# Kernel optimization log

Measured on AMD Instinct MI355X. Metric: run time of the kernel, lower is better.

Reference implementation:

```python
import jax, jax.numpy as jnp
import numpy as np
import itertools
from jax import lax

B, CIN, COUT, RES, NH = 32, 512, 512, 56, 8
STRIDE = RES // 7  # 8 -> post-stride grid is 7x7 (N=49)
HD = COUT // NH    # 64


def _affine(x, s, b):  # BatchNorm2d in inference form (per-channel scale/shift)
    return x * s[None, :, None, None] + b[None, :, None, None]


def _conv1x1(x, w):  # w: [O, C]
    return jnp.einsum('oc,bchw->bohw', w, x)


def _conv3x3(x, w, stride, groups):
    return lax.conv_general_dilated(
        x, w, window_strides=(stride, stride), padding=[(1, 1), (1, 1)],
        feature_group_count=groups, dimension_numbers=('NCHW', 'OIHW', 'NCHW'))


def _bias_idx():
    points = list(itertools.product(range(7), range(7)))
    offsets, idxs = {}, []
    for p1 in points:
        for p2 in points:
            off = (abs(p1[0] - p2[0]), abs(p1[1] - p2[1]))
            if off not in offsets:
                offsets[off] = len(offsets)
            idxs.append(offsets[off])
    return np.array(idxs, dtype=np.int32).reshape(49, 49), len(offsets)


def setup_inputs() -> dict:
    key = jax.random.key(0)
    ks = jax.random.split(key, 24)
    idx_np, n_off = _bias_idx()  # n_off = 49
    rn = lambda k, sh, sc: jax.random.normal(k, sh, dtype=jnp.float32) * sc
    return {
        'x': rn(ks[0], (B, CIN, RES, RES), 1.0),
        'dw_w': rn(ks[1], (CIN, 1, 3, 3), 0.2),
        'bn0_s': 1.0 + rn(ks[2], (CIN,), 0.05), 'bn0_b': rn(ks[3], (CIN,), 0.05),
        'wq': rn(ks[4], (COUT, CIN), 0.03),
        'bnq_s': 1.0 + rn(ks[5], (COUT,), 0.05), 'bnq_b': rn(ks[6], (COUT,), 0.05),
        'wk': rn(ks[7], (COUT, CIN), 0.03),
        'bnk_s': 1.0 + rn(ks[8], (COUT,), 0.05), 'bnk_b': rn(ks[9], (COUT,), 0.05),
        'wv': rn(ks[10], (COUT, CIN), 0.03),
        'bnv_s': 1.0 + rn(ks[11], (COUT,), 0.05), 'bnv_b': rn(ks[12], (COUT,), 0.05),
        'loc_w': rn(ks[13], (COUT, COUT // NH, 3, 3), 0.05), 'loc_b': rn(ks[14], (COUT,), 0.02),
        'bnl_s': 1.0 + rn(ks[15], (COUT,), 0.05), 'bnl_b': rn(ks[16], (COUT,), 0.05),
        'th1': rn(ks[17], (NH, NH), 0.3), 'th2': rn(ks[18], (NH, NH), 0.3),
        'logit_scale': jnp.log(10.0) * jnp.ones((NH, 1, 1), dtype=jnp.float32),
        'ab': rn(ks[19], (NH, n_off), 0.02),
        'wo': rn(ks[20], (COUT, COUT), 0.03),
        'bno_s': 1.0 + rn(ks[21], (COUT,), 0.05), 'bno_b': rn(ks[22], (COUT,), 0.05),
        'bias_idx': jnp.array(idx_np),
    }


def reference(x, dw_w, bn0_s, bn0_b, wq, bnq_s, bnq_b, wk, bnk_s, bnk_b,
              wv, bnv_s, bnv_b, loc_w, loc_b, bnl_s, bnl_b, th1, th2,
              logit_scale, ab, wo, bno_s, bno_b, bias_idx):
    # stride_conv: depthwise 3x3 stride-8 + BN -> [B, C, 7, 7]
    x = _affine(_conv3x3(x, dw_w, STRIDE, CIN), bn0_s, bn0_b)
    Bc, C, H, W = x.shape
    N = H * W  # 49
    q = _affine(_conv1x1(x, wq), bnq_s, bnq_b).reshape(Bc, NH, HD, N).transpose(0, 1, 3, 2)  # [B,H,N,d]
    k = _affine(_conv1x1(x, wk), bnk_s, bnk_b).reshape(Bc, NH, HD, N)                        # [B,H,d,N]
    v4 = _affine(_conv1x1(x, wv), bnv_s, bnv_b)                                              # [B,Cout,7,7]
    v_local = _affine(_conv3x3(v4, loc_w, 1, NH) + loc_b[None, :, None, None], bnl_s, bnl_b)
    v = v4.reshape(Bc, NH, HD, N).transpose(0, 1, 3, 2)                                      # [B,H,N,d]
    # faithful to source: q normalized over head_dim, k normalized over token axis (last)
    qn = q / jnp.maximum(jnp.linalg.norm(q, axis=-1, keepdims=True), 1e-12)
    kn = k / jnp.maximum(jnp.linalg.norm(k, axis=-1, keepdims=True), 1e-12)
    ls = jnp.exp(jnp.minimum(logit_scale, jnp.log(100.0)))  # clamp max then exp
    attn = jnp.einsum('bhnd,bhdm->bhnm', qn, kn) * ls + ab[:, bias_idx]  # [B,H,49,49]
    attn = jnp.einsum('ij,bjnm->binm', th1, attn)   # talking head 1
    attn = jax.nn.softmax(attn, axis=-1)
    attn = jnp.einsum('ij,bjnm->binm', th2, attn)   # talking head 2
    out = jnp.einsum('bhnm,bhmd->bhnd', attn, v)    # [B,H,N,d]
    out = out.transpose(0, 1, 3, 2).reshape(Bc, COUT, H, W) + v_local
    out = jax.image.resize(out, (Bc, COUT, H * STRIDE, W * STRIDE), method='bilinear')
    out = out * jax.nn.relu6(out + 3.0) / 6.0       # Hardswish
    return _affine(_conv1x1(out, wo), bno_s, bno_b)
```

## Files before the change

### kernel.cpp

```cpp
#include <hip/hip_runtime.h>
#include <hip/hip_bf16.h>
#include <stdint.h>

typedef short short8 __attribute__((ext_vector_type(8)));
typedef float f32x4 __attribute__((ext_vector_type(4)));

#define NB    32
#define NC    512
#define NHD   8
#define HDD   64
#define N7    49
#define RES   56
#define P56   3136
#define NTOK  1568
#define NTOKP 1664
#define NBIG  100352
#define KDIM  512
#define KLOC  576

__device__ __forceinline__ void gload_lds16(const __hip_bfloat16* g, __hip_bfloat16* l) {
  __builtin_amdgcn_global_load_lds(
      (const __attribute__((address_space(1))) void*)g,
      (__attribute__((address_space(3))) void*)l, 16, 0, 0);
}

__global__ __launch_bounds__(256) void k_cvt(
    const float* __restrict__ s0, const float* __restrict__ s1,
    const float* __restrict__ s2, const float* __restrict__ s3,
    const float* __restrict__ s4,
    __hip_bfloat16* __restrict__ d0, __hip_bfloat16* __restrict__ d1,
    __hip_bfloat16* __restrict__ d2, __hip_bfloat16* __restrict__ d3,
    __hip_bfloat16* __restrict__ d4) {
  const float* s; __hip_bfloat16* d; int n = NC * NC;
  switch (blockIdx.y) {
    case 0: s = s0; d = d0; break;
    case 1: s = s1; d = d1; break;
    case 2: s = s2; d = d2; break;
    case 3: s = s3; d = d3; break;
    default: s = s4; d = d4; n = NC * KLOC; break;
  }
  for (int i = blockIdx.x * blockDim.x + threadIdx.x; i < n; i += gridDim.x * blockDim.x)
    d[i] = __float2bfloat16(s[i]);
}

__global__ __launch_bounds__(64) void k_stride(
    const float* __restrict__ x, const float* __restrict__ dw,
    const float* __restrict__ s0, const float* __restrict__ b0,
    __hip_bfloat16* __restrict__ xs) {
  const int ci = blockIdx.x, b = blockIdx.y, t = threadIdx.x;
  __shared__ float rows[21][56];
  const float* xp = x + ((size_t)(b * NC + ci)) * RES * RES;
  for (int r = t; r < 21 * 56; r += 64) {
    int rr = r / 56, cc = r - rr * 56;
    int oh = rr / 3, kh = rr - oh * 3;
    int ih = oh * 8 + kh - 1;
    rows[rr][cc] = (ih >= 0) ? xp[ih * 56 + cc] : 0.f;
  }
  float w[9];
#pragma unroll
  for (int j = 0; j < 9; ++j) w[j] = dw[ci * 9 + j];
  const float sc = s0[ci], bi = b0[ci];
  __syncthreads();
  if (t < 49) {
    const int oh = t / 7, ow = t - oh * 7;
    float acc = 0.f;
#pragma unroll
    for (int kh = 0; kh < 3; ++kh)
#pragma unroll
      for (int kw = 0; kw < 3; ++kw) {
        int col = ow * 8 + kw - 1;
        float v = (col >= 0) ? rows[oh * 3 + kh][col] : 0.f;
        acc += v * w[kh * 3 + kw];
      }
    xs[(size_t)(b * 49 + t) * NC + ci] = __float2bfloat16(acc * sc + bi);
  }
}

__global__ __launch_bounds__(512) void k_gemm_big(
    const __hip_bfloat16* __restrict__ A,
    const __hip_bfloat16* __restrict__ Bm,
    const float* __restrict__ scale, const float* __restrict__ bias,
    float* __restrict__ out) {
  __shared__ __align__(16) __hip_bfloat16 lsA[4][256 * 32];
  __shared__ __align__(16) __hip_bfloat16 lsB[4][256 * 32];
  const int t = threadIdx.x;
  const int cpx = gridDim.x >> 3;
  const int nid = (blockIdx.x & 7) * cpx + (blockIdx.x >> 3);
  const int m0 = (nid & 1) * 256, n0 = (nid >> 1) * 256;

  const int lane = t & 63, wid = t >> 6;
  const int wm = (wid >> 2) * 128, wn = (wid & 3) * 64;
  const int fr = lane & 15, fq = lane >> 4;
  const int rslot = (fq ^ ((fr >> 1) & 3)) * 8;

  const int srow = t >> 2;
  const int scol = ((t & 3) ^ ((t >> 3) & 3)) * 8;
  const __hip_bfloat16* Ab = A  + (size_t)(m0 + srow) * KDIM + scol;
  const __hip_bfloat16* Bb = Bm + (size_t)(n0 + srow) * KDIM + scol;

  const f32x4 fz = {0.f, 0.f, 0.f, 0.f};
  f32x4 acc[8][4];
#pragma unroll
  for (int i = 0; i < 8; ++i)
#pragma unroll
    for (int j = 0; j < 4; ++j) acc[i][j] = fz;

#define STA(tile, call) gload_lds16(Ab + (tile) * 32 + (size_t)(call) * 128 * KDIM, \
                                    lsA[(tile) & 3] + (call) * 4096 + wid * 512)
#define STB(tile, call) gload_lds16(Bb + (tile) * 32 + (size_t)(call) * 128 * KDIM, \
                                    lsB[(tile) & 3] + (call) * 4096 + wid * 512)

  STA(0, 0); STA(0, 1); STB(0, 0); STB(0, 1);
  STA(1, 0); STA(1, 1); STB(1, 0); STB(1, 1);
  asm volatile("s_waitcnt vmcnt(4)" ::: "memory");
  __builtin_amdgcn_sched_barrier(0);
  __builtin_amdgcn_s_barrier();
  __builtin_amdgcn_sched_barrier(0);

#pragma unroll 1
  for (int tt = 0; tt < 16; ++tt) {
    const __hip_bfloat16* lA = lsA[tt & 3];
    const __hip_bfloat16* lB = lsB[tt & 3];
    const int ft = tt + 2;

    short8 af[4], bf[4], ag[4];
#pragma unroll
    for (int i = 0; i < 4; ++i)
      af[i] = *(const short8*)(lA + (wm + i * 16 + fr) * 32 + rslot);
#pragma unroll
    for (int j = 0; j < 4; ++j)
      bf[j] = *(const short8*)(lB + (wn + j * 16 + fr) * 32 + rslot);
    if (ft < 16) { STA(ft, 0); STA(ft, 1); }
    __builtin_amdgcn_sched_barrier(0);
    __builtin_amdgcn_s_barrier();
    asm volatile("s_waitcnt lgkmcnt(0)" ::: "memory");
    __builtin_amdgcn_sched_barrier(0);
    __builtin_amdgcn_s_setprio(1);
#pragma unroll
    for (int i = 0; i < 4; ++i)
#pragma unroll
      for (int j = 0; j < 4; ++j)
        acc[i][j] = __builtin_amdgcn_mfma_f32_16x16x32_bf16(af[i], bf[j], acc[i][j], 0, 0, 0);
    __builtin_amdgcn_s_setprio(0);
    __builtin_amdgcn_sched_barrier(0);
    __builtin_amdgcn_s_barrier();
    __builtin_amdgcn_sched_barrier(0);

#pragma unroll
    for (int i = 0; i < 4; ++i)
      ag[i] = *(const short8*)(lA + (wm + 64 + i * 16 + fr) * 32 + rslot);
    if (ft < 16) { STB(ft, 0); STB(ft, 1); }
    __builtin_amdgcn_sched_barrier(0);
    __builtin_amdgcn_s_barrier();
    asm volatile("s_waitcnt lgkmcnt(0)" ::: "memory");
    __builtin_amdgcn_sched_barrier(0);
    __builtin_amdgcn_s_setprio(1);
#pragma unroll
    for (int i = 0; i < 4; ++i)
#pragma unroll
      for (int j = 0; j < 4; ++j)
        acc[4 + i][j] = __builtin_amdgcn_mfma_f32_16x16x32_bf16(ag[i], bf[j], acc[4 + i][j], 0, 0, 0);
    __builtin_amdgcn_s_setprio(0);
    __builtin_amdgcn_sched_barrier(0);

    if (tt < 14)      asm volatile("s_waitcnt vmcnt(4)" ::: "memory");
    else if (tt == 14) asm volatile("s_waitcnt vmcnt(0)" ::: "memory");
    __builtin_amdgcn_sched_barrier(0);
    __builtin_amdgcn_s_barrier();
    __builtin_amdgcn_sched_barrier(0);
  }
#undef STA
#undef STB

#pragma unroll
  for (int mi = 0; mi < 8; ++mi) {
#pragma unroll
    for (int ni = 0; ni < 4; ++ni) {
      const int gn = n0 + wn + ni * 16 + fr;
      const int outer = gn / P56;
      const int ii = gn - outer * P56;
#pragma unroll
      for (int r = 0; r < 4; ++r) {
        const int co = m0 + wm + mi * 16 + fq * 4 + r;
        out[((size_t)outer * NC + co) * P56 + ii] = acc[mi][ni][r] * scale[co] + bias[co];
      }
    }
  }
}

__global__ __launch_bounds__(256) void k_gemm_qkv(
    const __hip_bfloat16* __restrict__ wqb, const __hip_bfloat16* __restrict__ wkb,
    const __hip_bfloat16* __restrict__ wvb, const __hip_bfloat16* __restrict__ xs,
    const float* __restrict__ sq, const float* __restrict__ bq,
    const float* __restrict__ sk, const float* __restrict__ bk,
    const float* __restrict__ sv, const float* __restrict__ bv,
    float* __restrict__ qb, float* __restrict__ kb, float* __restrict__ vb) {
  __shared__ __align__(16) __hip_bfloat16 la[2][128 * 32];
  __shared__ __align__(16) __hip_bfloat16 lb[2][128 * 32];
  const int t = threadIdx.x;
  const int nwg = gridDim.x;
  const int orig = blockIdx.x;
  const int q = nwg >> 3, r = nwg & 7;
  const int xcd = orig & 7, pos = orig >> 3;
  const int nid = (xcd < r ? xcd * (q + 1) : r * (q + 1) + (xcd - r) * q) + pos;
  const int mt = nid % 12, nt = nid / 12;
  const int n0 = nt * 128, m0 = (mt & 3) * 128, sel = mt >> 2;

  const __hip_bfloat16* A = (sel == 0 ? wqb : sel == 1 ? wkb : wvb);
  const float* scale = (sel == 0 ? sq : sel == 1 ? sk : sv);
  const float* bias  = (sel == 0 ? bq : sel == 1 ? bk : bv);
  float* out = (sel == 0 ? qb : sel == 1 ? kb : vb);

  const int lane = t & 63, wid = t >> 6;
  const int wm = (wid >> 1) * 64, wn = (wid & 1) * 64;
  const int fr = lane & 15, fq = lane >> 4, kg = fq * 8;
  const int rA0 = wid * 16;
  const int grow = lane >> 2;
  const int gcol = (lane & 3) * 8;

  const f32x4 fz = {0.f, 0.f, 0.f, 0.f};
  f32x4 acc[4][4];
#pragma unroll
  for (int i = 0; i < 4; ++i)
#pragma unroll
    for (int j = 0; j < 4; ++j) acc[i][j] = fz;

  const __hip_bfloat16* Ab = A + (size_t)(m0 + rA0 + grow) * KDIM + gcol;
  const __hip_bfloat16* Bb = xs + (size_t)(n0 + rA0 + grow) * KDIM + gcol;

#define STAGE_QKV(buf, k0)                                        \
  do {                                                            \
    gload_lds16(Ab + (k0),             la[buf] + rA0 * 32);       \
    gload_lds16(Ab + (k0) + 64 * KDIM, la[buf] + (rA0 + 64) * 32);\
    gload_lds16(Bb + (k0),             lb[buf] + rA0 * 32);       \
    gload_lds16(Bb + (k0) + 64 * KDIM, lb[buf] + (rA0 + 64) * 32);\
  } while (0)

  STAGE_QKV(0, 0);
  STAGE_QKV(1, 32);
  int cur = 0;
#pragma unroll 1
  for (int it = 0; it < 16; ++it) {
    if (it < 15) asm volatile("s_waitcnt vmcnt(4)" ::: "memory");
    else         asm volatile("s_waitcnt vmcnt(0)" ::: "memory");
    __builtin_amdgcn_sched_barrier(0);
    __builtin_amdgcn_s_barrier();
    __builtin_amdgcn_sched_barrier(0);
    const __hip_bfloat16* lap = la[cur];
    const __hip_bfloat16* lbp = lb[cur];
    short8 af[4], bf[4];
#pragma unroll
    for (int mi = 0; mi < 4; ++mi) af[mi] = *(const short8*)(lap + (wm + mi * 16 + fr) * 32 + kg);
#pragma unroll
    for (int ni = 0; ni < 4; ++ni) bf[ni] = *(const short8*)(lbp + (wn + ni * 16 + fr) * 32 + kg);
#pragma unroll
    for (int mi = 0; mi < 4; ++mi)
#pragma unroll
      for (int ni = 0; ni < 4; ++ni)
        acc[mi][ni] = __builtin_amdgcn_mfma_f32_16x16x32_bf16(af[mi], bf[ni], acc[mi][ni], 0, 0, 0);
    __builtin_amdgcn_sched_barrier(0);
    __builtin_amdgcn_s_barrier();
    __builtin_amdgcn_sched_barrier(0);
    if (it < 14) STAGE_QKV(cur, (it + 2) * 32);
    cur ^= 1;
  }
#undef STAGE_QKV

#pragma unroll
  for (int mi = 0; mi < 4; ++mi) {
#pragma unroll
    for (int ni = 0; ni < 4; ++ni) {
      const int gn = n0 + wn + ni * 16 + fr;
      if (gn >= NTOK) continue;
      const int b = gn / 49, ii = gn - b * 49;
#pragma unroll
      for (int r = 0; r < 4; ++r) {
        const int co = m0 + wm + mi * 16 + fq * 4 + r;
        out[((size_t)b * NC + co) * 49 + ii] = acc[mi][ni][r] * scale[co] + bias[co];
      }
    }
  }
}

__global__ __launch_bounds__(256) void k_im2col(
    const float* __restrict__ vb, __hip_bfloat16* __restrict__ bloc) {
  const int g = blockIdx.x, b = blockIdx.y, t = threadIdx.x;
  __shared__ __hip_bfloat16 pad[64][81];
  for (int i = t; i < 64 * 81; i += 256) pad[i / 81][i % 81] = __float2bfloat16(0.f);
  __syncthreads();
  const float* src = vb + ((size_t)b * NC + g * 64) * 49;
  for (int i = t; i < 64 * 49; i += 256) {
    const int ci = i / 49, n = i - ci * 49;
    const int oh = n / 7, ow = n - oh * 7;
    pad[ci][(oh + 1) * 9 + (ow + 1)] = __float2bfloat16(src[i]);
  }
  __syncthreads();
  __hip_bfloat16* dst = bloc + ((size_t)g * NTOK + (size_t)b * 49) * KLOC;
  for (int i = t; i < 49 * KLOC; i += 256) {
    const int n = i / KLOC, k = i - n * KLOC;
    const int ci = k / 9, tap = k - ci * 9;
    const int kh = tap / 3, kw = tap - kh * 3;
    const int oh = n / 7, ow = n - oh * 7;
    dst[i] = pad[ci][(oh + kh) * 9 + (ow + kw)];
  }
}

__global__ __launch_bounds__(256) void k_vloc_gemm(
    const __hip_bfloat16* __restrict__ lwb,
    const __hip_bfloat16* __restrict__ bloc,
    const float* __restrict__ lbias, const float* __restrict__ sl,
    const float* __restrict__ bl, float* __restrict__ vloc) {
  __shared__ __align__(16) unsigned short la[64][40];
  __shared__ __align__(16) unsigned short lb[128][40];
  const int t = threadIdx.x;
  const int g = blockIdx.y;
  const int n0 = blockIdx.x * 128;
  const int lane = t & 63, wid = t >> 6;
  const int wm = (wid >> 1) * 32, wn = (wid & 1) * 64;
  const int fr = lane & 15, fq = lane >> 4, kg = fq * 8;

  const f32x4 fz = {0.f, 0.f, 0.f, 0.f};
  f32x4 acc[2][4];
#pragma unroll
  for (int i = 0; i < 2; ++i)
#pragma unroll
    for (int j = 0; j < 4; ++j) acc[i][j] = fz;

  const int r0 = t >> 2, kk = (t & 3) * 8;
  const short8 z8 = {0, 0, 0, 0, 0, 0, 0, 0};
  const __hip_bfloat16* As = lwb + (size_t)g * 64 * KLOC;
  const __hip_bfloat16* Bs = bloc + (size_t)g * NTOK * KLOC;

  for (int k0 = 0; k0 < KLOC; k0 += 32) {
    __syncthreads();
    *(short8*)(&la[r0][kk]) = *(const short8*)(As + (size_t)r0 * KLOC + k0 + kk);
#pragma unroll
    for (int rr = 0; rr < 128; rr += 64) {
      const int row = r0 + rr;
      const int gn = n0 + row;
      short8 vb8 = z8;
      if (gn < NTOK) vb8 = *(const short8*)(Bs + (size_t)gn * KLOC + k0 + kk);
      *(short8*)(&lb[row][kk]) = vb8;
    }
    __syncthreads();
    short8 af[2], bfv[4];
#pragma unroll
    for (int mi = 0; mi < 2; ++mi) af[mi] = *(const short8*)(&la[wm + mi * 16 + fr][kg]);
#pragma unroll
    for (int ni = 0; ni < 4; ++ni) bfv[ni] = *(const short8*)(&lb[wn + ni * 16 + fr][kg]);
#pragma unroll
    for (int mi = 0; mi < 2; ++mi)
#pragma unroll
      for (int ni = 0; ni < 4; ++ni)
        acc[mi][ni] = __builtin_amdgcn_mfma_f32_16x16x32_bf16(af[mi], bfv[ni], acc[mi][ni], 0, 0, 0);
  }

#pragma unroll
  for (int mi = 0; mi < 2; ++mi) {
#pragma unroll
    for (int ni = 0; ni < 4; ++ni) {
      const int gn = n0 + wn + ni * 16 + fr;
      if (gn >= NTOK) continue;
      const int b = gn / 49, n = gn - b * 49;
#pragma unroll
      for (int r = 0; r < 4; ++r) {
        const int oc = g * 64 + wm + mi * 16 + fq * 4 + r;
        const float sc = sl[oc];
        vloc[((size_t)b * NC + oc) * 49 + n] = acc[mi][ni][r] * sc + lbias[oc] * sc + bl[oc];
      }
    }
  }
}

__global__ __launch_bounds__(256) void k_attn1(
    const float* __restrict__ qb, const float* __restrict__ kb,
    const float* __restrict__ lsc, const float* __restrict__ ab, const int* __restrict__ bidx,
    float* __restrict__ Sbuf) {
  const int h = blockIdx.x, b = blockIdx.y, t = threadIdx.x;
  __shared__ float qt[64 * 49], kt[64 * 49], nq[49], abl[49];
  const float* qs = qb + ((size_t)b * NC + h * 64) * 49;
  const float* ks = kb + ((size_t)b * NC + h * 64) * 49;
  for (int i = t; i < 64 * 49; i += 256) { qt[i] = qs[i]; kt[i] = ks[i]; }
  if (t < 49) abl[t] = ab[h * 49 + t];
  __syncthreads();
  if (t < 49) {
    float s = 0.f;
    for (int d = 0; d < 64; ++d) { float v = qt[d * 49 + t]; s += v * v; }
    nq[t] = fmaxf(sqrtf(s), 1e-12f);
  } else if (t >= 64 && t < 128) {
    const int d = t - 64;
    float s = 0.f;
    for (int m = 0; m < 49; ++m) { float v = kt[d * 49 + m]; s += v * v; }
    const float inv = 1.f / fmaxf(sqrtf(s), 1e-12f);
    for (int m = 0; m < 49; ++m) kt[d * 49 + m] *= inv;
  }
  __syncthreads();
  const float ls = expf(fminf(lsc[h], logf(100.f)));
  for (int idx = t; idx < 49 * 49; idx += 256) {
    const int n = idx / 49, m = idx - n * 49;
    float acc = 0.f;
    for (int d = 0; d < 64; ++d) acc += qt[d * 49 + n] * kt[d * 49 + m];
    Sbuf[(((size_t)b * NHD + h) * 49 + n) * 49 + m] = acc / nq[n] * ls + abl[bidx[idx]];
  }
}

__global__ __launch_bounds__(256) void k_attn2(
    const float* __restrict__ Sbuf, const float* __restrict__ th1, const float* __restrict__ th2,
    const float* __restrict__ vb, const float* __restrict__ vloc, float* __restrict__ y7) {
  const int n = blockIdx.x, b = blockIdx.y, t = threadIdx.x;
  __shared__ float sS[8][49], sP[8][49], sQ[8][49];
  __shared__ float t1[64], t2[64], rsuminv[8];
  if (t < 64) { t1[t] = th1[t]; t2[t] = th2[t]; }
  for (int i = t; i < 392; i += 256) {
    const int j = i / 49, m = i - j * 49;
    sS[j][m] = Sbuf[(((size_t)b * NHD + j) * 49 + n) * 49 + m];
  }
  __syncthreads();
  for (int i = t; i < 392; i += 256) {
    const int j = i / 49, m = i - j * 49;
    float a = 0.f;
#pragma unroll
    for (int jj = 0; jj < 8; ++jj) a += t1[j * 8 + jj] * sS[jj][m];
    sP[j][m] = a;
  }
  __syncthreads();
  if (t < 8) {
    float mx = -1e30f;
    for (int m = 0; m < 49; ++m) mx = fmaxf(mx, sP[t][m]);
    float s = 0.f;
    for (int m = 0; m < 49; ++m) { float e = expf(sP[t][m] - mx); sP[t][m] = e; s += e; }
    rsuminv[t] = 1.f / s;
  }
  __syncthreads();
  for (int i = t; i < 392; i += 256) {
    const int j = i / 49, m = i - j * 49;
    float a = 0.f;
#pragma unroll
    for (int jj = 0; jj < 8; ++jj) a += t2[j * 8 + jj] * (sP[jj][m] * rsuminv[jj]);
    sQ[j][m] = a;
  }
  __syncthreads();
  for (int c = t; c < NC; c += 256) {
    const int hh = c >> 6;
    const float* vp = vb + ((size_t)b * NC + c) * 49;
    float a = 0.f;
    for (int m = 0; m < 49; ++m) a += sQ[hh][m] * vp[m];
    a += vloc[((size_t)b * NC + c) * 49 + n];
    y7[((size_t)b * 49 + n) * NC + c] = a;
  }
}

__global__ __launch_bounds__(256) void k_resize(const float* __restrict__ y7,
                                                __hip_bfloat16* __restrict__ h) {
  const int y = blockIdx.x, b = blockIdx.y, t = threadIdx.x;
  __shared__ float L[2][7][512];
  float sy = (y - 3.5f) * 0.125f;
  sy = fminf(fmaxf(sy, 0.f), 6.f);
  const int iy0 = min((int)floorf(sy), 5);
  const float wy = sy - (float)iy0;
  const float* src = y7 + ((size_t)b * 49 + iy0 * 7) * NC;
  float* Lf = &L[0][0][0];
  for (int i = t; i < 2 * 7 * 512; i += 256) Lf[i] = src[i];
  __syncthreads();
  const size_t outb = ((size_t)b * P56 + (size_t)y * 56) * NC;
  const int c0 = t * 2;
  for (int x = 0; x < 56; ++x) {
    float sx = (x - 3.5f) * 0.125f;
    sx = fminf(fmaxf(sx, 0.f), 6.f);
    const int ix0 = min((int)floorf(sx), 5);
    const float wx = sx - (float)ix0;
    const float w00 = (1.f - wy) * (1.f - wx), w01 = (1.f - wy) * wx;
    const float w10 = wy * (1.f - wx),         w11 = wy * wx;
    float hs[2];
#pragma unroll
    for (int j = 0; j < 2; ++j) {
      const int c = c0 + j;
      const float v = w00 * L[0][ix0][c] + w01 * L[0][ix0 + 1][c]
                    + w10 * L[1][ix0][c] + w11 * L[1][ix0 + 1][c];
      hs[j] = v * fminf(fmaxf(v + 3.f, 0.f), 6.f) * (1.f / 6.f);
    }
    __hip_bfloat162 p;
    p.x = __float2bfloat16(hs[0]);
    p.y = __float2bfloat16(hs[1]);
    *(__hip_bfloat162*)(&h[outb + (size_t)x * NC + c0]) = p;
  }
}

extern "C" void kernel_launch(void* const* d_in, const int* in_sizes, int n_in,
                              void* d_out, int out_size, void* d_ws, size_t ws_size,
                              hipStream_t stream) {
  (void)in_sizes; (void)n_in; (void)out_size; (void)ws_size;
  const float* x     = (const float*)d_in[0];
  const float* dw_w  = (const float*)d_in[1];
  const float* bn0_s = (const float*)d_in[2];
  const float* bn0_b = (const float*)d_in[3];
  const float* wq    = (const float*)d_in[4];
  const float* bnq_s = (const float*)d_in[5];
  const float* bnq_b = (const float*)d_in[6];
  const float* wk    = (const float*)d_in[7];
  const float* bnk_s = (const float*)d_in[8];
  const float* bnk_b = (const float*)d_in[9];
  const float* wv    = (const float*)d_in[10];
  const float* bnv_s = (const float*)d_in[11];
  const float* bnv_b = (const float*)d_in[12];
  const float* loc_w = (const float*)d_in[13];
  const float* loc_b = (const float*)d_in[14];
  const float* bnl_s = (const float*)d_in[15];
  const float* bnl_b = (const float*)d_in[16];
  const float* th1   = (const float*)d_in[17];
  const float* th2   = (const float*)d_in[18];
  const float* lsc   = (const float*)d_in[19];
  const float* ab    = (const float*)d_in[20];
  const float* wo    = (const float*)d_in[21];
  const float* bno_s = (const float*)d_in[22];
  const float* bno_b = (const float*)d_in[23];
  const int*   bidx  = (const int*)d_in[24];

  char* w = (char*)d_ws;
  auto alloc = [&](size_t bytes) {
    char* p = w;
    w += (bytes + 255) & ~(size_t)255;
    return p;
  };
  __hip_bfloat16* h_buf = (__hip_bfloat16*)alloc((size_t)NBIG * NC * 2);
  __hip_bfloat16* wq_b  = (__hip_bfloat16*)alloc((size_t)NC * NC * 2);
  __hip_bfloat16* wk_b  = (__hip_bfloat16*)alloc((size_t)NC * NC * 2);
  __hip_bfloat16* wv_b  = (__hip_bfloat16*)alloc((size_t)NC * NC * 2);
  __hip_bfloat16* wo_b  = (__hip_bfloat16*)alloc((size_t)NC * NC * 2);
  __hip_bfloat16* lw_b  = (__hip_bfloat16*)alloc((size_t)NC * KLOC * 2);
  __hip_bfloat16* xs    = (__hip_bfloat16*)alloc((size_t)NTOKP * NC * 2);
  float* qb   = (float*)alloc((size_t)NB * NC * 49 * 4);
  float* kb   = (float*)alloc((size_t)NB * NC * 49 * 4);
  float* vb   = (float*)alloc((size_t)NB * NC * 49 * 4);
  float* vloc = (float*)alloc((size_t)NB * NC * 49 * 4);
  float* y7   = (float*)alloc((size_t)NB * 49 * NC * 4);
  float* Sb   = (float*)alloc((size_t)NB * NHD * 49 * 49 * 4);
  __hip_bfloat16* bloc = (__hip_bfloat16*)h_buf;

  k_cvt<<<dim3(128, 5), 256, 0, stream>>>(wq, wk, wv, wo, loc_w,
                                          wq_b, wk_b, wv_b, wo_b, lw_b);
  k_stride<<<dim3(NC, NB), 64, 0, stream>>>(x, dw_w, bn0_s, bn0_b, xs);
  k_gemm_qkv<<<dim3(13 * 12), 256, 0, stream>>>(wq_b, wk_b, wv_b, xs,
                                                bnq_s, bnq_b, bnk_s, bnk_b, bnv_s, bnv_b,
                                                qb, kb, vb);
  k_im2col<<<dim3(NHD, NB), 256, 0, stream>>>(vb, bloc);
  k_vloc_gemm<<<dim3(13, NHD), 256, 0, stream>>>(lw_b, bloc, loc_b, bnl_s, bnl_b, vloc);
  k_attn1<<<dim3(NHD, NB), 256, 0, stream>>>(qb, kb, lsc, ab, bidx, Sb);
  k_attn2<<<dim3(49, NB), 256, 0, stream>>>(Sb, th1, th2, vb, vloc, y7);
  k_resize<<<dim3(RES, NB), 256, 0, stream>>>(y7, h_buf);
  k_gemm_big<<<dim3(784), 512, 0, stream>>>(wo_b, h_buf, bno_s, bno_b, (float*)d_out);
}
```

Measured before the change: 272.5 us.

## Fuse stride/convert kernels, swizzle QKV LDS, pipeline local-conv GEMM with direct loads

Merges the weight bf16 conversion and the strided depthwise conv into one launch, with four channels per 256-thread block. Adds an XOR swizzle to the QKV GEMM's LDS layout to cut bank conflicts. Rewrites the local-conv GEMM to use double-buffered global-to-LDS direct loads with a padded token stride (NTOKP), in place of synchronous register staging with bounds checks. Removing the bounds check relies on the padded bloc rows beyond NTOK being readable; they may hold garbage, but those output columns are discarded.

```diff
diff --git a/kernel.cpp b/kernel.cpp
--- a/kernel.cpp
+++ b/kernel.cpp
@@ -24,55 +24,60 @@
       (__attribute__((address_space(3))) void*)l, 16, 0, 0);
 }
 
-__global__ __launch_bounds__(256) void k_cvt(
-    const float* __restrict__ s0, const float* __restrict__ s1,
-    const float* __restrict__ s2, const float* __restrict__ s3,
-    const float* __restrict__ s4,
+__global__ __launch_bounds__(256) void k_stride_cvt(
+    const float* __restrict__ x, const float* __restrict__ dw,
+    const float* __restrict__ s0, const float* __restrict__ b0,
+    __hip_bfloat16* __restrict__ xs,
+    const float* __restrict__ c0, const float* __restrict__ c1,
+    const float* __restrict__ c2, const float* __restrict__ c3,
+    const float* __restrict__ c4,
     __hip_bfloat16* __restrict__ d0, __hip_bfloat16* __restrict__ d1,
     __hip_bfloat16* __restrict__ d2, __hip_bfloat16* __restrict__ d3,
     __hip_bfloat16* __restrict__ d4) {
-  const float* s; __hip_bfloat16* d; int n = NC * NC;
-  switch (blockIdx.y) {
-    case 0: s = s0; d = d0; break;
-    case 1: s = s1; d = d1; break;
-    case 2: s = s2; d = d2; break;
-    case 3: s = s3; d = d3; break;
-    default: s = s4; d = d4; n = NC * KLOC; break;
-  }
-  for (int i = blockIdx.x * blockDim.x + threadIdx.x; i < n; i += gridDim.x * blockDim.x)
-    d[i] = __float2bfloat16(s[i]);
-}
-
-__global__ __launch_bounds__(64) void k_stride(
-    const float* __restrict__ x, const float* __restrict__ dw,
-    const float* __restrict__ s0, const float* __restrict__ b0,
-    __hip_bfloat16* __restrict__ xs) {
-  const int ci = blockIdx.x, b = blockIdx.y, t = threadIdx.x;
-  __shared__ float rows[21][56];
+  const int bid = blockIdx.x, t = threadIdx.x;
+  if (bid >= 4096) {
+    const long base = (long)(bid - 4096) * 2048;
+#pragma unroll
+    for (int j = 0; j < 8; ++j) {
+      long i = base + t + j * 256;
+      const float* s; __hip_bfloat16* d; long off;
+      if (i >= 1048576)      { s = c4; d = d4; off = i - 1048576; }
+      else if (i >= 786432)  { s = c3; d = d3; off = i - 786432; }
+      else if (i >= 524288)  { s = c2; d = d2; off = i - 524288; }
+      else if (i >= 262144)  { s = c1; d = d1; off = i - 262144; }
+      else                   { s = c0; d = d0; off = i; }
+      d[off] = __float2bfloat16(s[off]);
+    }
+    return;
+  }
+  const int b = bid >> 7, cig = bid & 127;
+  const int sub = t >> 6, lane = t & 63;
+  const int ci = cig * 4 + sub;
+  __shared__ float rows[4][21][56];
   const float* xp = x + ((size_t)(b * NC + ci)) * RES * RES;
-  for (int r = t; r < 21 * 56; r += 64) {
+  for (int r = lane; r < 21 * 56; r += 64) {
     int rr = r / 56, cc = r - rr * 56;
     int oh = rr / 3, kh = rr - oh * 3;
     int ih = oh * 8 + kh - 1;
-    rows[rr][cc] = (ih >= 0) ? xp[ih * 56 + cc] : 0.f;
+    rows[sub][rr][cc] = (ih >= 0) ? xp[ih * 56 + cc] : 0.f;
   }
   float w[9];
 #pragma unroll
   for (int j = 0; j < 9; ++j) w[j] = dw[ci * 9 + j];
   const float sc = s0[ci], bi = b0[ci];
   __syncthreads();
-  if (t < 49) {
-    const int oh = t / 7, ow = t - oh * 7;
+  if (lane < 49) {
+    const int oh = lane / 7, ow = lane - oh * 7;
     float acc = 0.f;
 #pragma unroll
     for (int kh = 0; kh < 3; ++kh)
 #pragma unroll
       for (int kw = 0; kw < 3; ++kw) {
         int col = ow * 8 + kw - 1;
-        float v = (col >= 0) ? rows[oh * 3 + kh][col] : 0.f;
+        float v = (col >= 0) ? rows[sub][oh * 3 + kh][col] : 0.f;
         acc += v * w[kh * 3 + kw];
       }
-    xs[(size_t)(b * 49 + t) * NC + ci] = __float2bfloat16(acc * sc + bi);
+    xs[(size_t)(b * 49 + lane) * NC + ci] = __float2bfloat16(acc * sc + bi);
   }
 }
 
@@ -195,8 +200,8 @@
     const float* __restrict__ sk, const float* __restrict__ bk,
     const float* __restrict__ sv, const float* __restrict__ bv,
     float* __restrict__ qb, float* __restrict__ kb, float* __restrict__ vb) {
-  __shared__ __align__(16) __hip_bfloat16 la[2][128 * 32];
-  __shared__ __align__(16) __hip_bfloat16 lb[2][128 * 32];
+  __shared__ __align__(16) __hip_bfloat16 lsA[2][128 * 32];
+  __shared__ __align__(16) __hip_bfloat16 lsB[2][128 * 32];
   const int t = threadIdx.x;
   const int nwg = gridDim.x;
   const int orig = blockIdx.x;
@@ -213,10 +218,12 @@
 
   const int lane = t & 63, wid = t >> 6;
   const int wm = (wid >> 1) * 64, wn = (wid & 1) * 64;
-  const int fr = lane & 15, fq = lane >> 4, kg = fq * 8;
-  const int rA0 = wid * 16;
-  const int grow = lane >> 2;
-  const int gcol = (lane & 3) * 8;
+  const int fr = lane & 15, fq = lane >> 4;
+  const int rslot = (fq ^ ((fr >> 1) & 3)) * 8;
+  const int srow = t >> 2;
+  const int scol = ((t & 3) ^ ((t >> 3) & 3)) * 8;
+  const __hip_bfloat16* Ab = A  + (size_t)(m0 + srow) * KDIM + scol;
+  const __hip_bfloat16* Bb = xs + (size_t)(n0 + srow) * KDIM + scol;
 
   const f32x4 fz = {0.f, 0.f, 0.f, 0.f};
   f32x4 acc[4][4];
@@ -225,20 +232,17 @@
 #pragma unroll
     for (int j = 0; j < 4; ++j) acc[i][j] = fz;
 
-  const __hip_bfloat16* Ab = A + (size_t)(m0 + rA0 + grow) * KDIM + gcol;
-  const __hip_bfloat16* Bb = xs + (size_t)(n0 + rA0 + grow) * KDIM + gcol;
-
-#define STAGE_QKV(buf, k0)                                        \
-  do {                                                            \
-    gload_lds16(Ab + (k0),             la[buf] + rA0 * 32);       \
-    gload_lds16(Ab + (k0) + 64 * KDIM, la[buf] + (rA0 + 64) * 32);\
-    gload_lds16(Bb + (k0),             lb[buf] + rA0 * 32);       \
-    gload_lds16(Bb + (k0) + 64 * KDIM, lb[buf] + (rA0 + 64) * 32);\
+#define STG_QKV(tile)                                                   \
+  do {                                                                  \
+    const int kof = (tile) * 32; const int bb = (tile) & 1;             \
+    gload_lds16(Ab + kof,                       lsA[bb] + wid * 512);   \
+    gload_lds16(Ab + kof + (size_t)64 * KDIM,   lsA[bb] + 2048 + wid * 512); \
+    gload_lds16(Bb + kof,                       lsB[bb] + wid * 512);   \
+    gload_lds16(Bb + kof + (size_t)64 * KDIM,   lsB[bb] + 2048 + wid * 512); \
   } while (0)
 
-  STAGE_QKV(0, 0);
-  STAGE_QKV(1, 32);
-  int cur = 0;
+  STG_QKV(0);
+  STG_QKV(1);
 #pragma unroll 1
   for (int it = 0; it < 16; ++it) {
     if (it < 15) asm volatile("s_waitcnt vmcnt(4)" ::: "memory");
@@ -246,13 +250,15 @@
     __builtin_amdgcn_sched_barrier(0);
     __builtin_amdgcn_s_barrier();
     __builtin_amdgcn_sched_barrier(0);
-    const __hip_bfloat16* lap = la[cur];
-    const __hip_bfloat16* lbp = lb[cur];
+    const __hip_bfloat16* lA = lsA[it & 1];
+    const __hip_bfloat16* lB = lsB[it & 1];
     short8 af[4], bf[4];
 #pragma unroll
-    for (int mi = 0; mi < 4; ++mi) af[mi] = *(const short8*)(lap + (wm + mi * 16 + fr) * 32 + kg);
-#pragma unroll
-    for (int ni = 0; ni < 4; ++ni) bf[ni] = *(const short8*)(lbp + (wn + ni * 16 + fr) * 32 + kg);
+    for (int mi = 0; mi < 4; ++mi)
+      af[mi] = *(const short8*)(lA + (wm + mi * 16 + fr) * 32 + rslot);
+#pragma unroll
+    for (int ni = 0; ni < 4; ++ni)
+      bf[ni] = *(const short8*)(lB + (wn + ni * 16 + fr) * 32 + rslot);
 #pragma unroll
     for (int mi = 0; mi < 4; ++mi)
 #pragma unroll
@@ -261,10 +267,9 @@
     __builtin_amdgcn_sched_barrier(0);
     __builtin_amdgcn_s_barrier();
     __builtin_amdgcn_sched_barrier(0);
-    if (it < 14) STAGE_QKV(cur, (it + 2) * 32);
-    cur ^= 1;
-  }
-#undef STAGE_QKV
+    if (it < 14) STG_QKV(it + 2);
+  }
+#undef STG_QKV
 
 #pragma unroll
   for (int mi = 0; mi < 4; ++mi) {
@@ -295,7 +300,7 @@
     pad[ci][(oh + 1) * 9 + (ow + 1)] = __float2bfloat16(src[i]);
   }
   __syncthreads();
-  __hip_bfloat16* dst = bloc + ((size_t)g * NTOK + (size_t)b * 49) * KLOC;
+  __hip_bfloat16* dst = bloc + ((size_t)g * NTOKP + (size_t)b * 49) * KLOC;
   for (int i = t; i < 49 * KLOC; i += 256) {
     const int n = i / KLOC, k = i - n * KLOC;
     const int ci = k / 9, tap = k - ci * 9;
@@ -310,14 +315,19 @@
     const __hip_bfloat16* __restrict__ bloc,
     const float* __restrict__ lbias, const float* __restrict__ sl,
     const float* __restrict__ bl, float* __restrict__ vloc) {
-  __shared__ __align__(16) unsigned short la[64][40];
-  __shared__ __align__(16) unsigned short lb[128][40];
+  __shared__ __align__(16) __hip_bfloat16 lsA[2][64 * 32];
+  __shared__ __align__(16) __hip_bfloat16 lsB[2][128 * 32];
   const int t = threadIdx.x;
   const int g = blockIdx.y;
   const int n0 = blockIdx.x * 128;
   const int lane = t & 63, wid = t >> 6;
   const int wm = (wid >> 1) * 32, wn = (wid & 1) * 64;
-  const int fr = lane & 15, fq = lane >> 4, kg = fq * 8;
+  const int fr = lane & 15, fq = lane >> 4;
+  const int rslot = (fq ^ ((fr >> 1) & 3)) * 8;
+  const int srow = t >> 2;
+  const int scol = ((t & 3) ^ ((t >> 3) & 3)) * 8;
+  const __hip_bfloat16* Ab = lwb  + ((size_t)g * 64 + srow) * KLOC + scol;
+  const __hip_bfloat16* Bb = bloc + ((size_t)g * NTOKP + n0 + srow) * KLOC + scol;
 
   const f32x4 fz = {0.f, 0.f, 0.f, 0.f};
   f32x4 acc[2][4];
@@ -326,34 +336,43 @@
 #pragma unroll
     for (int j = 0; j < 4; ++j) acc[i][j] = fz;
 
-  const int r0 = t >> 2, kk = (t & 3) * 8;
-  const short8 z8 = {0, 0, 0, 0, 0, 0, 0, 0};
-  const __hip_bfloat16* As = lwb + (size_t)g * 64 * KLOC;
-  const __hip_bfloat16* Bs = bloc + (size_t)g * NTOK * KLOC;
-
-  for (int k0 = 0; k0 < KLOC; k0 += 32) {
-    __syncthreads();
-    *(short8*)(&la[r0][kk]) = *(const short8*)(As + (size_t)r0 * KLOC + k0 + kk);
-#pragma unroll
-    for (int rr = 0; rr < 128; rr += 64) {
-      const int row = r0 + rr;
-      const int gn = n0 + row;
-      short8 vb8 = z8;
-      if (gn < NTOK) vb8 = *(const short8*)(Bs + (size_t)gn * KLOC + k0 + kk);
-      *(short8*)(&lb[row][kk]) = vb8;
-    }
-    __syncthreads();
-    short8 af[2], bfv[4];
-#pragma unroll
-    for (int mi = 0; mi < 2; ++mi) af[mi] = *(const short8*)(&la[wm + mi * 16 + fr][kg]);
-#pragma unroll
-    for (int ni = 0; ni < 4; ++ni) bfv[ni] = *(const short8*)(&lb[wn + ni * 16 + fr][kg]);
+#define STG_VL(tile)                                                     \
+  do {                                                                   \
+    const int kof = (tile) * 32; const int bb = (tile) & 1;              \
+    gload_lds16(Ab + kof,                      lsA[bb] + wid * 512);     \
+    gload_lds16(Bb + kof,                      lsB[bb] + wid * 512);     \
+    gload_lds16(Bb + kof + (size_t)64 * KLOC,  lsB[bb] + 2048 + wid * 512); \
+  } while (0)
+
+  STG_VL(0);
+  STG_VL(1);
+#pragma unroll 1
+  for (int it = 0; it < 18; ++it) {
+    if (it < 17) asm volatile("s_waitcnt vmcnt(3)" ::: "memory");
+    else         asm volatile("s_waitcnt vmcnt(0)" ::: "memory");
+    __builtin_amdgcn_sched_barrier(0);
+    __builtin_amdgcn_s_barrier();
+    __builtin_amdgcn_sched_barrier(0);
+    const __hip_bfloat16* lA = lsA[it & 1];
+    const __hip_bfloat16* lB = lsB[it & 1];
+    short8 af[2], bf[4];
 #pragma unroll
     for (int mi = 0; mi < 2; ++mi)
+      af[mi] = *(const short8*)(lA + (wm + mi * 16 + fr) * 32 + rslot);
+#pragma unroll
+    for (int ni = 0; ni < 4; ++ni)
+      bf[ni] = *(const short8*)(lB + (wn + ni * 16 + fr) * 32 + rslot);
+#pragma unroll
+    for (int mi = 0; mi < 2; ++mi)
 #pragma unroll
       for (int ni = 0; ni < 4; ++ni)
-        acc[mi][ni] = __builtin_amdgcn_mfma_f32_16x16x32_bf16(af[mi], bfv[ni], acc[mi][ni], 0, 0, 0);
-  }
+        acc[mi][ni] = __builtin_amdgcn_mfma_f32_16x16x32_bf16(af[mi], bf[ni], acc[mi][ni], 0, 0, 0);
+    __builtin_amdgcn_sched_barrier(0);
+    __builtin_amdgcn_s_barrier();
+    __builtin_amdgcn_sched_barrier(0);
+    if (it < 16) STG_VL(it + 2);
+  }
+#undef STG_VL
 
 #pragma unroll
   for (int mi = 0; mi < 2; ++mi) {
@@ -537,9 +556,9 @@
   float* Sb   = (float*)alloc((size_t)NB * NHD * 49 * 49 * 4);
   __hip_bfloat16* bloc = (__hip_bfloat16*)h_buf;
 
-  k_cvt<<<dim3(128, 5), 256, 0, stream>>>(wq, wk, wv, wo, loc_w,
-                                          wq_b, wk_b, wv_b, wo_b, lw_b);
-  k_stride<<<dim3(NC, NB), 64, 0, stream>>>(x, dw_w, bn0_s, bn0_b, xs);
+  k_stride_cvt<<<dim3(4096 + 656), 256, 0, stream>>>(
+      x, dw_w, bn0_s, bn0_b, xs,
+      wq, wk, wv, wo, loc_w, wq_b, wk_b, wv_b, wo_b, lw_b);
   k_gemm_qkv<<<dim3(13 * 12), 256, 0, stream>>>(wq_b, wk_b, wv_b, xs,
                                                 bnq_s, bnq_b, bnk_s, bnk_b, bnv_s, bnv_b,
                                                 qb, kb, vb);
```

Measured after the change: 262.5 us. 3.7% less time.
